# Performance work log

Measured on AMD Instinct MI355X. Metric: run time of the kernel, lower is better.

Reference implementation:

```python
import jax, jax.numpy as jnp
import numpy as np

B, L, D = 32, 512, 1024          # batch, seq_len, bert_dim
M, T, S = 8, 2, 4                # answer lists, texts, disjoint spans per text
NEG = -1e7                       # replace_masked_values fill used by the module


def setup_inputs() -> dict:
    key = jax.random.key(0)
    ks = jax.random.split(key, 8)
    return {
        "bert_out": jax.random.normal(ks[0], (B, L, D), jnp.float32),
        "seq_mask": jnp.ones((B, L), jnp.int32),
        "wordpiece_mask": jnp.ones((B, L), jnp.int32),
        "answer_as_text_to_disjoint_bios": jax.random.randint(ks[1], (B, T, S, L), 0, 3),
        "answer_as_list_of_bios": jax.random.randint(ks[2], (B, M, L), 0, 3),
        "span_bio_labels": jax.random.randint(ks[3], (B, L), 0, 3),
        "is_bio_mask": jnp.ones((B,), jnp.int32),
        # predictor = Linear(D, D) -> ReLU -> (Dropout, eval) -> Linear(D, 3)
        "W1": jax.random.normal(ks[4], (D, D), jnp.float32) / np.sqrt(D),
        "b1": jnp.zeros((D,), jnp.float32),
        "W2": jax.random.normal(ks[5], (D, 3), jnp.float32) / np.sqrt(D),
        "b2": jnp.zeros((3,), jnp.float32),
    }


def reference(bert_out, seq_mask, wordpiece_mask, answer_as_text_to_disjoint_bios,
              answer_as_list_of_bios, span_bio_labels, is_bio_mask,
              W1, b1, W2, b2):
    # ---- module(): FF predictor + masked log-softmax ----
    h = jax.nn.relu(jnp.einsum("bld,dh->blh", bert_out, W1) + b1)
    logits = jnp.einsum("blh,hc->blc", h, W2) + b2            # (B, L, 3)
    log_probs = jax.nn.log_softmax(logits, axis=-1)
    log_probs = log_probs * seq_mask[:, :, None].astype(log_probs.dtype)  # masked -> 0.0

    # ---- log_likelihood(), generation_top_k == 0 branch ----
    ab = answer_as_list_of_bios * seq_mask[:, None, :]        # (B, M, L)
    is_pregen = (ab.sum((1, 2)) > 0).astype(jnp.int32)        # (B,)
    extra = (span_bio_labels * (1 - is_pregen)[:, None])[:, None, :]  # (B, 1, L)
    list_of_bios = jnp.concatenate([ab, extra], axis=1)       # (B, M+1, L)

    # ---- _get_combined_likelihood: gather tag log-probs per candidate sequence ----
    ll = jnp.take_along_axis(log_probs[:, None], list_of_bios[..., None], axis=-1)[..., 0]  # (B, M+1, L)
    pad = list_of_bios.sum(-1) > 0                             # (B, M+1) non-empty sequences
    ll = ll * pad[..., None]
    seq_ll = jnp.where(pad, ll.sum(-1), NEG)                   # (B, M+1)
    lml = jax.nn.logsumexp(seq_ll, axis=-1)                    # (B,)
    return jnp.where(is_bio_mask.astype(bool), lml, NEG)
```

## Files before the change

kernel.cpp:

```cpp
#include <hip/hip_runtime.h>
#include <hip/hip_bf16.h>
#include <cstdint>

#define GLOBAL_AS __attribute__((address_space(1)))
#define LDS_AS    __attribute__((address_space(3)))

typedef short s8v  __attribute__((ext_vector_type(8)));
typedef float f4v  __attribute__((ext_vector_type(4)));
typedef unsigned short u8s __attribute__((ext_vector_type(8)));

#define NEGV (-1e7f)

__device__ __forceinline__ void gload_lds16(const void* g, void* l) {
  __builtin_amdgcn_global_load_lds((const GLOBAL_AS uint32_t*)g,
                                   (LDS_AS uint32_t*)l, 16, 0, 0);
}

__device__ __forceinline__ unsigned short f2bf(float f) {
  union { float f; uint32_t u; } v; v.f = f;
  uint32_t u = v.u;
  u += 0x7fffu + ((u >> 16) & 1u);
  return (unsigned short)(u >> 16);
}

__global__ __launch_bounds__(256) void cvt_a(const float* __restrict__ x,
                                             unsigned short* __restrict__ y,
                                             int n8) {
  int i = blockIdx.x * blockDim.x + threadIdx.x;
  int stride = gridDim.x * blockDim.x;
  for (; i < n8; i += stride) {
    float4 a = ((const float4*)x)[2 * i + 0];
    float4 b = ((const float4*)x)[2 * i + 1];
    u8s o;
    o[0] = f2bf(a.x); o[1] = f2bf(a.y); o[2] = f2bf(a.z); o[3] = f2bf(a.w);
    o[4] = f2bf(b.x); o[5] = f2bf(b.y); o[6] = f2bf(b.z); o[7] = f2bf(b.w);
    ((u8s*)y)[i] = o;
  }
}

__global__ __launch_bounds__(256) void cvt_w1t(const float* __restrict__ w1,
                                               unsigned short* __restrict__ w1t) {
  __shared__ float tile[32][33];
  int bx = blockIdx.x & 31;
  int by = blockIdx.x >> 5;
  int tx = threadIdx.x & 31;
  int ty = threadIdx.x >> 5;
#pragma unroll
  for (int j = 0; j < 4; ++j) {
    int kk = ty + j * 8;
    tile[kk][tx] = w1[(size_t)(by * 32 + kk) * 1024 + bx * 32 + tx];
  }
  __syncthreads();
#pragma unroll
  for (int j = 0; j < 4; ++j) {
    int nn = ty + j * 8;
    w1t[(size_t)(bx * 32 + nn) * 1024 + by * 32 + tx] = f2bf(tile[tx][nn]);
  }
}

__global__ __launch_bounds__(512, 2) void gemm_fused(
    const unsigned short* __restrict__ Abf,
    const unsigned short* __restrict__ Bbf,
    const float* __restrict__ b1,
    const float* __restrict__ W2,
    float* __restrict__ partials)
{
  __shared__ __align__(16) char lds[147456];

  int bid = blockIdx.x;
  int wid = (bid & 7) * 32 + (bid >> 3);
  int mt = wid >> 2;
  int nt = wid & 3;

  int tid  = threadIdx.x;
  int lane = tid & 63;
  int wv   = tid >> 6;
  int wr   = wv >> 2;
  int wc   = wv & 3;

  int laneq = lane & 15;
  int klo   = (lane >> 4) << 4;
  int sw    = (laneq & 7) << 4;
  int x0    = klo ^ sw;
  int x1    = (64 + klo) ^ sw;

  const size_t arow0 = (size_t)mt * 256;
  const size_t brow0 = (size_t)nt * 256;

  int scol = ((lane & 7) * 16) ^ ((lane >> 3) << 4);
  const unsigned short* gA = Abf + (arow0 + (lane >> 3)) * 1024 + (scol >> 1)
                                 + (size_t)wv * 16 * 1024;
  const unsigned short* gB = Bbf + (brow0 + (lane >> 3)) * 1024 + (scol >> 1)
                                 + (size_t)wv * 16 * 1024;

  f4v acc[8][4];
#pragma unroll
  for (int m = 0; m < 8; ++m)
#pragma unroll
    for (int n = 0; n < 4; ++n)
      acc[m][n] = f4v{0.f, 0.f, 0.f, 0.f};

  s8v a_frag[4][2];
  s8v b_frag[2][2][2];

  auto STAGE = [&](int ts, int isB, int rh) {
    int ok  = ts < 16;
    int tcl = ok ? ts : 15;
    const unsigned short* g = (isB ? gB : gA) + (size_t)rh * 128 * 1024 + tcl * 64;
    int dst = ok ? (((tcl & 1) << 16) | (isB << 15) | (rh << 14) | (wv << 11))
                 : (131072 + (wv << 11));
    gload_lds16(g,            lds + dst);
    gload_lds16(g + 8 * 1024, lds + dst + 1024);
  };

  auto READ_A = [&](int buf, int mq) {
    const char* p = lds + (buf << 16) + (wr << 14) + laneq * 128 + mq * 8192;
#pragma unroll
    for (int m = 0; m < 4; ++m) {
      a_frag[m][0] = *(const s8v*)(p + m * 2048 + x0);
      a_frag[m][1] = *(const s8v*)(p + m * 2048 + x1);
    }
  };
  auto READ_B = [&](int buf, int np) {
    const char* p = lds + (buf << 16) + 32768 + ((wc >> 1) << 14)
                        + ((wc & 1) * 64 + laneq) * 128 + np * 4096;
#pragma unroll
    for (int n2 = 0; n2 < 2; ++n2) {
      b_frag[np][n2][0] = *(const s8v*)(p + n2 * 2048 + x0);
      b_frag[np][n2][1] = *(const s8v*)(p + n2 * 2048 + x1);
    }
  };
  auto MFMA_Q = [&](int mq, int np) {
    __builtin_amdgcn_s_setprio(1);
#pragma unroll
    for (int m = 0; m < 4; ++m)
#pragma unroll
      for (int n2 = 0; n2 < 2; ++n2) {
        acc[mq*4+m][np*2+n2] = __builtin_amdgcn_mfma_f32_16x16x32_bf16(
            a_frag[m][0], b_frag[np][n2][0], acc[mq*4+m][np*2+n2], 0, 0, 0);
        acc[mq*4+m][np*2+n2] = __builtin_amdgcn_mfma_f32_16x16x32_bf16(
            a_frag[m][1], b_frag[np][n2][1], acc[mq*4+m][np*2+n2], 0, 0, 0);
      }
    __builtin_amdgcn_s_setprio(0);
  };

#define BAR  __builtin_amdgcn_s_barrier()
#define SB0  __builtin_amdgcn_sched_barrier(0)
#define VM4  asm volatile("s_waitcnt vmcnt(4)" ::: "memory")

  STAGE(0,1,0); STAGE(0,0,0); STAGE(0,0,1); STAGE(0,1,1);
  STAGE(1,1,0); STAGE(1,0,0);
  VM4; BAR;

  for (int i = 0; i < 8; ++i) {
    int T = 2 * i;
    READ_A(0,0); READ_B(0,0); STAGE(T+1,0,1);
    BAR; SB0; MFMA_Q(0,0); SB0; BAR;
    READ_B(0,1);             STAGE(T+1,1,1);
    BAR; SB0; MFMA_Q(0,1); SB0; BAR;
    READ_A(0,1);             STAGE(T+2,1,0);
    BAR; SB0; MFMA_Q(1,1); SB0; BAR;
                             STAGE(T+2,0,0);
    VM4;
    BAR; SB0; MFMA_Q(1,0); SB0; BAR;
    READ_A(1,0); READ_B(1,0); STAGE(T+2,0,1);
    BAR; SB0; MFMA_Q(0,0); SB0; BAR;
    READ_B(1,1);             STAGE(T+2,1,1);
    BAR; SB0; MFMA_Q(0,1); SB0; BAR;
    READ_A(1,1);             STAGE(T+3,1,0);
    BAR; SB0; MFMA_Q(1,1); SB0; BAR;
                             STAGE(T+3,0,0);
    VM4;
    BAR; SB0; MFMA_Q(1,0); SB0; BAR;
  }

#undef BAR
#undef SB0
#undef VM4

  float b1v[4];
  float w2v[4][3];
#pragma unroll
  for (int n = 0; n < 4; ++n) {
    int gc = nt * 256 + wc * 64 + n * 16 + laneq;
    b1v[n] = b1[gc];
    w2v[n][0] = W2[gc * 3 + 0];
    w2v[n][1] = W2[gc * 3 + 1];
    w2v[n][2] = W2[gc * 3 + 2];
  }

  float* red = (float*)lds;
#pragma unroll
  for (int m = 0; m < 8; ++m) {
#pragma unroll
    for (int q = 0; q < 4; ++q) {
      float p0 = 0.f, p1 = 0.f, p2 = 0.f;
#pragma unroll
      for (int n = 0; n < 4; ++n) {
        float h = acc[m][n][q] + b1v[n];
        h = fmaxf(h, 0.f);
        p0 += h * w2v[n][0];
        p1 += h * w2v[n][1];
        p2 += h * w2v[n][2];
      }
#pragma unroll
      for (int s = 1; s < 16; s <<= 1) {
        p0 += __shfl_xor(p0, s, 64);
        p1 += __shfl_xor(p1, s, 64);
        p2 += __shfl_xor(p2, s, 64);
      }
      if ((lane & 15) == 0) {
        int row = wr * 128 + m * 16 + (lane >> 4) * 4 + q;
        red[(wc * 256 + row) * 3 + 0] = p0;
        red[(wc * 256 + row) * 3 + 1] = p1;
        red[(wc * 256 + row) * 3 + 2] = p2;
      }
    }
  }
  __syncthreads();
  if (tid < 256) {
    float s0 = 0.f, s1 = 0.f, s2 = 0.f;
#pragma unroll
    for (int w = 0; w < 4; ++w) {
      s0 += red[(w * 256 + tid) * 3 + 0];
      s1 += red[(w * 256 + tid) * 3 + 1];
      s2 += red[(w * 256 + tid) * 3 + 2];
    }
    size_t o = ((size_t)nt * 16384 + (size_t)mt * 256 + tid) * 3;
    partials[o + 0] = s0;
    partials[o + 1] = s1;
    partials[o + 2] = s2;
  }
}

__device__ __forceinline__ float blockReduceSum(float v, float* red, int t) {
#pragma unroll
  for (int s = 32; s >= 1; s >>= 1) v += __shfl_xor(v, s, 64);
  __syncthreads();
  if ((t & 63) == 0) red[t >> 6] = v;
  __syncthreads();
  return red[0] + red[1] + red[2] + red[3];
}

__global__ __launch_bounds__(256) void finalize(
    const float* __restrict__ partials,
    const float* __restrict__ b2,
    const int* __restrict__ seq_mask,
    const int* __restrict__ ans,
    const int* __restrict__ span,
    const int* __restrict__ isbio,
    float* __restrict__ out)
{
  int b = blockIdx.x;
  int t = threadIdx.x;
  __shared__ float lp[512][3];
  __shared__ float red[4];
  __shared__ float seq_ll[9];
  __shared__ int preg;

  float b20 = b2[0], b21 = b2[1], b22 = b2[2];
  const int NP = 16384 * 3;

  for (int l = t; l < 512; l += 256) {
    int gi = b * 512 + l;
    float x0 = b20, x1 = b21, x2 = b22;
#pragma unroll
    for (int w = 0; w < 4; ++w) {
      x0 += partials[w * NP + gi * 3 + 0];
      x1 += partials[w * NP + gi * 3 + 1];
      x2 += partials[w * NP + gi * 3 + 2];
    }
    float mx = fmaxf(x0, fmaxf(x1, x2));
    float lse = mx + logf(expf(x0 - mx) + expf(x1 - mx) + expf(x2 - mx));
    float msk = (float)seq_mask[gi];
    lp[l][0] = (x0 - lse) * msk;
    lp[l][1] = (x1 - lse) * msk;
    lp[l][2] = (x2 - lse) * msk;
  }
  __syncthreads();

  float s = 0.f;
  for (int i = t; i < 8 * 512; i += 256) {
    int m = i >> 9, l = i & 511;
    s += (float)(ans[(b * 8 + m) * 512 + l] * seq_mask[b * 512 + l]);
  }
  s = blockReduceSum(s, red, t);
  if (t == 0) preg = (s > 0.f) ? 1 : 0;
  __syncthreads();
  int ip = preg;

  for (int m = 0; m < 9; ++m) {
    float sll = 0.f, sidx = 0.f;
    for (int l = t; l < 512; l += 256) {
      int idx;
      if (m < 8) idx = ans[(b * 8 + m) * 512 + l] * seq_mask[b * 512 + l];
      else       idx = span[b * 512 + l] * (1 - ip);
      sll  += lp[l][idx];
      sidx += (float)idx;
    }
    sll  = blockReduceSum(sll, red, t);
    sidx = blockReduceSum(sidx, red, t);
    if (t == 0) seq_ll[m] = (sidx > 0.f) ? sll : NEGV;
  }

  if (t == 0) {
    float mx = seq_ll[0];
#pragma unroll
    for (int m = 1; m < 9; ++m) mx = fmaxf(mx, seq_ll[m]);
    float sum = 0.f;
#pragma unroll
    for (int m = 0; m < 9; ++m) sum += expf(seq_ll[m] - mx);
    float lml = mx + logf(sum);
    out[b] = isbio[b] ? lml : NEGV;
  }
}

extern "C" void kernel_launch(void* const* d_in, const int* in_sizes, int n_in,
                              void* d_out, int out_size, void* d_ws, size_t ws_size,
                              hipStream_t stream) {
  const float* bert     = (const float*)d_in[0];
  const int*   seq_mask = (const int*)d_in[1];
  const int*   ans      = (const int*)d_in[4];
  const int*   span     = (const int*)d_in[5];
  const int*   isbio    = (const int*)d_in[6];
  const float* W1       = (const float*)d_in[7];
  const float* b1       = (const float*)d_in[8];
  const float* W2       = (const float*)d_in[9];
  const float* b2       = (const float*)d_in[10];
  float* out = (float*)d_out;

  char* ws = (char*)d_ws;
  float* partials     = (float*)ws;
  unsigned short* Abf = (unsigned short*)(ws + (1 << 20));
  unsigned short* W1T = (unsigned short*)(ws + (1 << 20) + (size_t)16384 * 1024 * 2);

  cvt_a<<<2048, 256, 0, stream>>>(bert, Abf, 16384 * 1024 / 8);
  cvt_w1t<<<1024, 256, 0, stream>>>(W1, W1T);
  gemm_fused<<<256, 512, 0, stream>>>(Abf, W1T, b1, W2, partials);
  finalize<<<32, 256, 0, stream>>>(partials, b2, seq_mask, ans, span, isbio, out);
}
```

Baseline: 78.10 us.

## Fuse fp32-to-bf16 conversion of activations into GEMM A-tile loads

```diff
diff --git a/kernel.cpp b/kernel.cpp
--- a/kernel.cpp
+++ b/kernel.cpp
@@ -21,21 +21,6 @@
   uint32_t u = v.u;
   u += 0x7fffu + ((u >> 16) & 1u);
   return (unsigned short)(u >> 16);
-}
-
-__global__ __launch_bounds__(256) void cvt_a(const float* __restrict__ x,
-                                             unsigned short* __restrict__ y,
-                                             int n8) {
-  int i = blockIdx.x * blockDim.x + threadIdx.x;
-  int stride = gridDim.x * blockDim.x;
-  for (; i < n8; i += stride) {
-    float4 a = ((const float4*)x)[2 * i + 0];
-    float4 b = ((const float4*)x)[2 * i + 1];
-    u8s o;
-    o[0] = f2bf(a.x); o[1] = f2bf(a.y); o[2] = f2bf(a.z); o[3] = f2bf(a.w);
-    o[4] = f2bf(b.x); o[5] = f2bf(b.y); o[6] = f2bf(b.z); o[7] = f2bf(b.w);
-    ((u8s*)y)[i] = o;
-  }
 }
 
 __global__ __launch_bounds__(256) void cvt_w1t(const float* __restrict__ w1,
@@ -59,13 +44,13 @@
 }
 
 __global__ __launch_bounds__(512, 2) void gemm_fused(
-    const unsigned short* __restrict__ Abf,
+    const float* __restrict__ A32,
     const unsigned short* __restrict__ Bbf,
     const float* __restrict__ b1,
     const float* __restrict__ W2,
     float* __restrict__ partials)
 {
-  __shared__ __align__(16) char lds[147456];
+  __shared__ __align__(16) char lds[131072];
 
   int bid = blockIdx.x;
   int wid = (bid & 7) * 32 + (bid >> 3);
@@ -88,8 +73,7 @@
   const size_t brow0 = (size_t)nt * 256;
 
   int scol = ((lane & 7) * 16) ^ ((lane >> 3) << 4);
-  const unsigned short* gA = Abf + (arow0 + (lane >> 3)) * 1024 + (scol >> 1)
-                                 + (size_t)wv * 16 * 1024;
+  const float* gA32 = A32 + (arow0 + (size_t)wv * 16 + (lane >> 3)) * 1024 + (scol >> 1);
   const unsigned short* gB = Bbf + (brow0 + (lane >> 3)) * 1024 + (scol >> 1)
                                  + (size_t)wv * 16 * 1024;
 
@@ -102,15 +86,44 @@
 
   s8v a_frag[4][2];
   s8v b_frag[2][2][2];
-
-  auto STAGE = [&](int ts, int isB, int rh) {
-    int ok  = ts < 16;
-    int tcl = ok ? ts : 15;
-    const unsigned short* g = (isB ? gB : gA) + (size_t)rh * 128 * 1024 + tcl * 64;
-    int dst = ok ? (((tcl & 1) << 16) | (isB << 15) | (rh << 14) | (wv << 11))
-                 : (131072 + (wv << 11));
-    gload_lds16(g,            lds + dst);
-    gload_lds16(g + 8 * 1024, lds + dst + 1024);
+  float4 areg[8];
+
+  auto A_LOAD = [&](int tt) {
+    const float* base = gA32 + tt * 64;
+#pragma unroll
+    for (int rh = 0; rh < 2; ++rh) {
+      const float* p = base + (size_t)rh * 128 * 1024;
+      areg[rh * 4 + 0] = *(const float4*)(p);
+      areg[rh * 4 + 1] = *(const float4*)(p + 4);
+      areg[rh * 4 + 2] = *(const float4*)(p + 8 * 1024);
+      areg[rh * 4 + 3] = *(const float4*)(p + 8 * 1024 + 4);
+    }
+  };
+  auto A_WRITE = [&](int tt) {
+    int buf = tt & 1;
+#pragma unroll
+    for (int rh = 0; rh < 2; ++rh) {
+      int dst = (buf << 16) | (rh << 14) | (wv << 11);
+#pragma unroll
+      for (int rr = 0; rr < 2; ++rr) {
+        float4 lo = areg[rh * 4 + rr * 2 + 0];
+        float4 hi = areg[rh * 4 + rr * 2 + 1];
+        u8s o;
+        o[0] = f2bf(lo.x); o[1] = f2bf(lo.y); o[2] = f2bf(lo.z); o[3] = f2bf(lo.w);
+        o[4] = f2bf(hi.x); o[5] = f2bf(hi.y); o[6] = f2bf(hi.z); o[7] = f2bf(hi.w);
+        *(u8s*)(lds + dst + rr * 1024 + lane * 16) = o;
+      }
+    }
+  };
+  auto STAGE_B = [&](int tt) {
+    const unsigned short* g = gB + tt * 64;
+#pragma unroll
+    for (int rh = 0; rh < 2; ++rh) {
+      int dst = ((tt & 1) << 16) | (1 << 15) | (rh << 14) | (wv << 11);
+      const unsigned short* p = g + (size_t)rh * 128 * 1024;
+      gload_lds16(p,            lds + dst);
+      gload_lds16(p + 8 * 1024, lds + dst + 1024);
+    }
   };
 
   auto READ_A = [&](int buf, int mq) {
@@ -146,37 +159,35 @@
 
 #define BAR  __builtin_amdgcn_s_barrier()
 #define SB0  __builtin_amdgcn_sched_barrier(0)
-#define VM4  asm volatile("s_waitcnt vmcnt(4)" ::: "memory")
-
-  STAGE(0,1,0); STAGE(0,0,0); STAGE(0,0,1); STAGE(0,1,1);
-  STAGE(1,1,0); STAGE(1,0,0);
-  VM4; BAR;
-
-  for (int i = 0; i < 8; ++i) {
-    int T = 2 * i;
-    READ_A(0,0); READ_B(0,0); STAGE(T+1,0,1);
-    BAR; SB0; MFMA_Q(0,0); SB0; BAR;
-    READ_B(0,1);             STAGE(T+1,1,1);
-    BAR; SB0; MFMA_Q(0,1); SB0; BAR;
-    READ_A(0,1);             STAGE(T+2,1,0);
-    BAR; SB0; MFMA_Q(1,1); SB0; BAR;
-                             STAGE(T+2,0,0);
-    VM4;
-    BAR; SB0; MFMA_Q(1,0); SB0; BAR;
-    READ_A(1,0); READ_B(1,0); STAGE(T+2,0,1);
-    BAR; SB0; MFMA_Q(0,0); SB0; BAR;
-    READ_B(1,1);             STAGE(T+2,1,1);
-    BAR; SB0; MFMA_Q(0,1); SB0; BAR;
-    READ_A(1,1);             STAGE(T+3,1,0);
-    BAR; SB0; MFMA_Q(1,1); SB0; BAR;
-                             STAGE(T+3,0,0);
-    VM4;
-    BAR; SB0; MFMA_Q(1,0); SB0; BAR;
+#define VM0  asm volatile("s_waitcnt vmcnt(0)" ::: "memory")
+#define LK0  asm volatile("s_waitcnt lgkmcnt(0)" ::: "memory")
+
+  A_LOAD(0);
+  STAGE_B(0);
+  A_WRITE(0);
+  VM0; LK0; SB0;
+  BAR;
+
+  for (int t = 0; t < 16; ++t) {
+    int c = t & 1;
+    bool pf = (t < 15);
+    if (pf) A_LOAD(t + 1);
+    READ_A(c, 0); READ_B(c, 0);
+    BAR; SB0; MFMA_Q(0, 0); SB0; BAR;
+    if (pf) STAGE_B(t + 1);
+    READ_B(c, 1);
+    BAR; SB0; MFMA_Q(0, 1); SB0; BAR;
+    READ_A(c, 1);
+    if (pf) A_WRITE(t + 1);
+    BAR; SB0; MFMA_Q(1, 1); SB0; BAR;
+    VM0; LK0; SB0;
+    BAR; SB0; MFMA_Q(1, 0); SB0; BAR;
   }
 
 #undef BAR
 #undef SB0
-#undef VM4
+#undef VM0
+#undef LK0
 
   float b1v[4];
   float w2v[4][3];
@@ -331,11 +342,9 @@
 
   char* ws = (char*)d_ws;
   float* partials     = (float*)ws;
-  unsigned short* Abf = (unsigned short*)(ws + (1 << 20));
-  unsigned short* W1T = (unsigned short*)(ws + (1 << 20) + (size_t)16384 * 1024 * 2);
-
-  cvt_a<<<2048, 256, 0, stream>>>(bert, Abf, 16384 * 1024 / 8);
+  unsigned short* W1T = (unsigned short*)(ws + (1 << 20));
+
   cvt_w1t<<<1024, 256, 0, stream>>>(W1, W1T);
-  gemm_fused<<<256, 512, 0, stream>>>(Abf, W1T, b1, W2, partials);
+  gemm_fused<<<256, 512, 0, stream>>>(bert, W1T, b1, W2, partials);
   finalize<<<32, 256, 0, stream>>>(partials, b2, seq_mask, ans, span, isbio, out);
 }
```

Measured after the change: 84.08 us. +7.7%, slower.
